# Kernel optimization log

Hardware: AMD Instinct MI355X
Metric: run time of the kernel (lower is better)

The kernel has to match this reference:

```python
import jax, jax.numpy as jnp
import numpy as np


def setup_inputs() -> dict:
    key = jax.random.key(0)
    ks = jax.random.split(key, 11)
    B, H, P, D, E = 64, 20, 448, 64, 1280
    s = 0.02
    return {
        "hidden_states": jax.random.normal(ks[0], (B, 1, E), jnp.float32),
        "past_k": jax.random.normal(ks[1], (B, H, P, D), jnp.float32),
        "past_v": jax.random.normal(ks[2], (B, H, P, D), jnp.float32),
        "past_keep_mask": jnp.zeros((1, 1, 1, P), jnp.float32),
        "Wq": jax.random.normal(ks[3], (E, E), jnp.float32) * s,
        "bq": jax.random.normal(ks[4], (E,), jnp.float32) * s,
        "Wk": jax.random.normal(ks[5], (E, E), jnp.float32) * s,
        "Wv": jax.random.normal(ks[6], (E, E), jnp.float32) * s,
        "bv": jax.random.normal(ks[7], (E,), jnp.float32) * s,
        "Wo": jax.random.normal(ks[8], (E, E), jnp.float32) * s,
        "bo": jax.random.normal(ks[9], (E,), jnp.float32) * s,
    }


def reference(hidden_states, past_k, past_v, past_keep_mask, Wq, bq, Wk, Wv, bv, Wo, bo):
    B, S, E = hidden_states.shape  # S == 1 (decode step)
    H, D = past_k.shape[1], past_k.shape[3]
    scale = jnp.asarray(D, jnp.float32) ** -0.5

    def split_heads(x):  # [B,S,E] -> [B,H,S,D]
        return x.reshape(B, S, H, D).transpose(0, 2, 1, 3)

    q = split_heads((hidden_states @ Wq.T + bq) * scale)
    new_k = split_heads(hidden_states @ Wk.T)
    new_v = split_heads(hidden_states @ Wv.T + bv)

    all_k = jnp.concatenate([past_k, new_k], axis=2)  # [B,H,P+1,D]
    all_v = jnp.concatenate([past_v, new_v], axis=2)
    mask = jnp.concatenate(
        [past_keep_mask, jnp.zeros((1, 1, 1, 1), past_keep_mask.dtype)], axis=-1
    )  # [1,1,1,P+1]

    attn = jnp.einsum("bhqd,bhkd->bhqk", q, all_k) + mask
    attn = jax.nn.softmax(attn, axis=-1)
    ctx = jnp.einsum("bhqk,bhkd->bhqd", attn, all_v)  # [B,H,S,D]
    merged = ctx.transpose(0, 2, 1, 3).reshape(B, S, E)
    out = merged @ Wo.T + bo
    return out, new_k, new_v
```

## Files before the change

### kernel.cpp

```cpp
#include <hip/hip_runtime.h>

#define EDIM 1280
#define BDIM 64
#define HDIM 20
#define PDIM 448
#define DDIM 64
#define NCOL 3840
#define NCHUNK 4
#define ECHUNK 320
#define CTILE 32

__device__ __forceinline__ float dot4(float4 a, float4 b) {
    return a.x * b.x + a.y * b.y + a.z * b.z + a.w * b.w;
}

__global__ __launch_bounds__(256) void proj_qkv(
    const float* __restrict__ h,
    const float* __restrict__ Wq, const float* __restrict__ Wk,
    const float* __restrict__ Wv,
    float* __restrict__ partial)
{
    __shared__ float Wt[CTILE * ECHUNK];

    const int wave = threadIdx.x >> 6;
    const int lane = threadIdx.x & 63;
    const int colbase = blockIdx.x * CTILE;
    const int e0 = blockIdx.y * ECHUNK;

    const float* W; int wc;
    if (colbase < EDIM)          { W = Wq; wc = colbase; }
    else if (colbase < 2 * EDIM) { W = Wk; wc = colbase - EDIM; }
    else                         { W = Wv; wc = colbase - 2 * EDIM; }

#pragma unroll
    for (int i = 0; i < 10; ++i) {
        int i4 = (i * 256 + threadIdx.x) * 4;
        int c  = i4 / ECHUNK;
        int e  = i4 - c * ECHUNK;
        *reinterpret_cast<float4*>(&Wt[i4]) =
            *reinterpret_cast<const float4*>(&W[(size_t)(wc + c) * EDIM + e0 + e]);
    }
    __syncthreads();

    float acc[8];
#pragma unroll
    for (int c = 0; c < 8; ++c) acc[c] = 0.f;

    const float4* hp = reinterpret_cast<const float4*>(h + lane * EDIM + e0);
    const int c0 = wave * 8;
#pragma unroll 4
    for (int eg = 0; eg < ECHUNK / 4; ++eg) {
        float4 hv = hp[eg];
#pragma unroll
        for (int c = 0; c < 8; ++c) {
            float4 wv = *reinterpret_cast<const float4*>(&Wt[(c0 + c) * ECHUNK + eg * 4]);
            acc[c] += dot4(hv, wv);
        }
    }
#pragma unroll
    for (int c = 0; c < 8; ++c)
        partial[((size_t)blockIdx.y * NCOL + colbase + c0 + c) * 64 + lane] = acc[c];
}

__global__ __launch_bounds__(256) void reduce_proj(
    const float* __restrict__ partial,
    const float* __restrict__ bq, const float* __restrict__ bv,
    float* __restrict__ qout, float* __restrict__ kout, float* __restrict__ vout)
{
    __shared__ float tile[256];
    const int cg0 = blockIdx.x * 4;
    const int idx = cg0 * 64 + threadIdx.x;
    float v = partial[idx] + partial[245760 + idx]
            + partial[491520 + idx] + partial[737280 + idx];
    tile[threadIdx.x] = v;
    __syncthreads();
    const int row = threadIdx.x >> 2;
    const int c   = threadIdx.x & 3;
    const int cg  = cg0 + c;
    const float v2 = tile[c * 64 + row];
    if (cg < EDIM)
        qout[row * EDIM + cg] = (v2 + bq[cg]) * 0.125f;
    else if (cg < 2 * EDIM)
        kout[row * EDIM + (cg - EDIM)] = v2;
    else
        vout[row * EDIM + (cg - 2 * EDIM)] = v2 + bv[cg - 2 * EDIM];
}

__global__ __launch_bounds__(256) void attn_decode(
    const float* __restrict__ q,
    const float* __restrict__ Kpast,
    const float* __restrict__ Vpast,
    const float* __restrict__ mask,
    const float* __restrict__ knew,
    const float* __restrict__ vnew,
    float* __restrict__ merged)
{
    __shared__ float sp[PDIM + 2];
    __shared__ float red[8];
    __shared__ float4 ctxp[4][16];

    const int bh = blockIdx.x;
    const int b  = bh / HDIM;
    const int hh = bh % HDIM;
    const int t  = threadIdx.x;
    const int w  = t >> 6;
    const int lane = t & 63;
    const int grp = t >> 4;
    const int dg  = t & 15;

    const float* qp = q + b * EDIM + hh * DDIM;
    const float* Kb = Kpast + (size_t)bh * PDIM * DDIM;
    const float* Vb = Vpast + (size_t)bh * PDIM * DDIM;
    const float* nk = knew + b * EDIM + hh * DDIM;
    const float* nv = vnew + b * EDIM + hh * DDIM;

    const float4 qv = *reinterpret_cast<const float4*>(qp + dg * 4);

    float lmax = -3.4e38f;
    for (int j0 = 0; j0 < PDIM; j0 += 64) {
        const int j = j0 + grp;
        float4 k0 = *reinterpret_cast<const float4*>(Kb + (size_t)j * DDIM + dg * 4);
        float4 k1 = *reinterpret_cast<const float4*>(Kb + (size_t)(j + 16) * DDIM + dg * 4);
        float4 k2 = *reinterpret_cast<const float4*>(Kb + (size_t)(j + 32) * DDIM + dg * 4);
        float4 k3 = *reinterpret_cast<const float4*>(Kb + (size_t)(j + 48) * DDIM + dg * 4);
        float s0 = dot4(qv, k0), s1 = dot4(qv, k1), s2 = dot4(qv, k2), s3 = dot4(qv, k3);
#pragma unroll
        for (int off = 8; off; off >>= 1) {
            s0 += __shfl_xor(s0, off, 16);
            s1 += __shfl_xor(s1, off, 16);
            s2 += __shfl_xor(s2, off, 16);
            s3 += __shfl_xor(s3, off, 16);
        }
        if (dg == 0) {
            s0 += mask[j]; s1 += mask[j + 16]; s2 += mask[j + 32]; s3 += mask[j + 48];
            sp[j] = s0; sp[j + 16] = s1; sp[j + 32] = s2; sp[j + 48] = s3;
            lmax = fmaxf(lmax, fmaxf(fmaxf(s0, s1), fmaxf(s2, s3)));
        }
    }
    if (grp == 0) {
        float4 kn = *reinterpret_cast<const float4*>(nk + dg * 4);
        float sn = dot4(qv, kn);
#pragma unroll
        for (int off = 8; off; off >>= 1) sn += __shfl_xor(sn, off, 16);
        if (dg == 0) { sp[PDIM] = sn; lmax = fmaxf(lmax, sn); }
    }
#pragma unroll
    for (int off = 32; off; off >>= 1) lmax = fmaxf(lmax, __shfl_xor(lmax, off, 64));
    if (lane == 0) red[w] = lmax;
    __syncthreads();
    const float mx = fmaxf(fmaxf(red[0], red[1]), fmaxf(red[2], red[3]));

    float lsum = 0.f;
    for (int j = t; j <= PDIM; j += 256) {
        float pj = __expf(sp[j] - mx);
        sp[j] = pj;
        lsum += pj;
    }
#pragma unroll
    for (int off = 32; off; off >>= 1) lsum += __shfl_xor(lsum, off, 64);
    if (lane == 0) red[4 + w] = lsum;
    __syncthreads();
    const float inv = 1.f / (red[4] + red[5] + red[6] + red[7]);

    const int kk = lane >> 4;
    const int dp = lane & 15;
    float4 acc = make_float4(0.f, 0.f, 0.f, 0.f);
    for (int j0 = 0; j0 < PDIM; j0 += 64) {
        const int jb = j0 + w * 16 + kk;
        float p0 = sp[jb], p1 = sp[jb + 4], p2 = sp[jb + 8], p3 = sp[jb + 12];
        float4 v0 = *reinterpret_cast<const float4*>(Vb + (size_t)jb * DDIM + dp * 4);
        float4 v1 = *reinterpret_cast<const float4*>(Vb + (size_t)(jb + 4) * DDIM + dp * 4);
        float4 v2 = *reinterpret_cast<const float4*>(Vb + (size_t)(jb + 8) * DDIM + dp * 4);
        float4 v3 = *reinterpret_cast<const float4*>(Vb + (size_t)(jb + 12) * DDIM + dp * 4);
        acc.x += p0 * v0.x + p1 * v1.x + p2 * v2.x + p3 * v3.x;
        acc.y += p0 * v0.y + p1 * v1.y + p2 * v2.y + p3 * v3.y;
        acc.z += p0 * v0.z + p1 * v1.z + p2 * v2.z + p3 * v3.z;
        acc.w += p0 * v0.w + p1 * v1.w + p2 * v2.w + p3 * v3.w;
    }
    if (w == 0 && kk == 0) {
        float pn = sp[PDIM];
        float4 vn = *reinterpret_cast<const float4*>(nv + dp * 4);
        acc.x += pn * vn.x; acc.y += pn * vn.y; acc.z += pn * vn.z; acc.w += pn * vn.w;
    }
    acc.x += __shfl_xor(acc.x, 16, 64); acc.y += __shfl_xor(acc.y, 16, 64);
    acc.z += __shfl_xor(acc.z, 16, 64); acc.w += __shfl_xor(acc.w, 16, 64);
    acc.x += __shfl_xor(acc.x, 32, 64); acc.y += __shfl_xor(acc.y, 32, 64);
    acc.z += __shfl_xor(acc.z, 32, 64); acc.w += __shfl_xor(acc.w, 32, 64);
    if (kk == 0) ctxp[w][dp] = acc;
    __syncthreads();
    if (t < 16) {
        float4 a0 = ctxp[0][t], a1 = ctxp[1][t], a2 = ctxp[2][t], a3 = ctxp[3][t];
        float4 r;
        r.x = (a0.x + a1.x + a2.x + a3.x) * inv;
        r.y = (a0.y + a1.y + a2.y + a3.y) * inv;
        r.z = (a0.z + a1.z + a2.z + a3.z) * inv;
        r.w = (a0.w + a1.w + a2.w + a3.w) * inv;
        *reinterpret_cast<float4*>(merged + b * EDIM + hh * DDIM + t * 4) = r;
    }
}

__global__ __launch_bounds__(256) void proj_out(
    const float* __restrict__ x,
    const float* __restrict__ Wo,
    float* __restrict__ partial)
{
    __shared__ float Wt[CTILE * ECHUNK];

    const int wave = threadIdx.x >> 6;
    const int lane = threadIdx.x & 63;
    const int colbase = blockIdx.x * CTILE;
    const int e0 = blockIdx.y * ECHUNK;

#pragma unroll
    for (int i = 0; i < 10; ++i) {
        int i4 = (i * 256 + threadIdx.x) * 4;
        int c  = i4 / ECHUNK;
        int e  = i4 - c * ECHUNK;
        *reinterpret_cast<float4*>(&Wt[i4]) =
            *reinterpret_cast<const float4*>(&Wo[(size_t)(colbase + c) * EDIM + e0 + e]);
    }
    __syncthreads();

    float acc[8];
#pragma unroll
    for (int c = 0; c < 8; ++c) acc[c] = 0.f;

    const float4* xp = reinterpret_cast<const float4*>(x + lane * EDIM + e0);
    const int c0 = wave * 8;
#pragma unroll 4
    for (int eg = 0; eg < ECHUNK / 4; ++eg) {
        float4 hv = xp[eg];
#pragma unroll
        for (int c = 0; c < 8; ++c) {
            float4 wv = *reinterpret_cast<const float4*>(&Wt[(c0 + c) * ECHUNK + eg * 4]);
            acc[c] += dot4(hv, wv);
        }
    }
#pragma unroll
    for (int c = 0; c < 8; ++c)
        partial[((size_t)blockIdx.y * EDIM + colbase + c0 + c) * 64 + lane] = acc[c];
}

__global__ __launch_bounds__(256) void reduce_out(
    const float* __restrict__ partial, const float* __restrict__ bo,
    float* __restrict__ out)
{
    __shared__ float tile[256];
    const int cg0 = blockIdx.x * 4;
    const int idx = cg0 * 64 + threadIdx.x;
    float v = partial[idx] + partial[81920 + idx]
            + partial[163840 + idx] + partial[245760 + idx];
    tile[threadIdx.x] = v;
    __syncthreads();
    const int row = threadIdx.x >> 2;
    const int c   = threadIdx.x & 3;
    const int cg  = cg0 + c;
    out[row * EDIM + cg] = tile[c * 64 + row] + bo[cg];
}

extern "C" void kernel_launch(void* const* d_in, const int* in_sizes, int n_in,
                              void* d_out, int out_size, void* d_ws, size_t ws_size,
                              hipStream_t stream)
{
    const float* h    = (const float*)d_in[0];
    const float* pk   = (const float*)d_in[1];
    const float* pv   = (const float*)d_in[2];
    const float* mask = (const float*)d_in[3];
    const float* Wq   = (const float*)d_in[4];
    const float* bq   = (const float*)d_in[5];
    const float* Wk   = (const float*)d_in[6];
    const float* Wv   = (const float*)d_in[7];
    const float* bv   = (const float*)d_in[8];
    const float* Wo   = (const float*)d_in[9];
    const float* bo   = (const float*)d_in[10];

    float* out  = (float*)d_out;
    float* kout = (float*)d_out + 81920;
    float* vout = (float*)d_out + 163840;

    float* ws    = (float*)d_ws;
    float* partP = ws;
    float* qbuf  = ws + 983040;
    float* mrg   = ws + 983040 + 81920;
    float* partO = ws + 983040 + 163840;

    proj_qkv<<<dim3(NCOL / CTILE, NCHUNK), 256, 0, stream>>>(h, Wq, Wk, Wv, partP);
    reduce_proj<<<dim3(NCOL / 4), 256, 0, stream>>>(partP, bq, bv, qbuf, kout, vout);
    attn_decode<<<dim3(BDIM * HDIM), 256, 0, stream>>>(qbuf, pk, pv, mask, kout, vout, mrg);
    proj_out<<<dim3(EDIM / CTILE, NCHUNK), 256, 0, stream>>>(mrg, Wo, partO);
    reduce_out<<<dim3(EDIM / 4), 256, 0, stream>>>(partO, bo, out);
}
```

Measured before the change: 97.30 us.

## Split decode attention into KV chunks with separate softmax combine kernel

Attention over the 448-entry past is split into 7 chunks of 64 keys, one block per (chunk, batch-head). Each block loads its K and V rows up front, computes a local max, exp-sum and unnormalized context, and writes them to workspace. A new combine kernel merges the chunk partials with the new-token score using log-sum-exp rescaling. This exposes seven times more blocks and more loads in flight to hide HBM latency, at the cost of an extra launch and a small partial-buffer round trip. The partial buffers reuse the projection workspace region.

```diff
diff --git a/kernel.cpp b/kernel.cpp
--- a/kernel.cpp
+++ b/kernel.cpp
@@ -9,6 +9,7 @@
 #define NCHUNK 4
 #define ECHUNK 320
 #define CTILE 32
+#define KCHUNKS 7
 
 __device__ __forceinline__ float dot4(float4 a, float4 b) {
     return a.x * b.x + a.y * b.y + a.z * b.z + a.w * b.w;
@@ -86,20 +87,20 @@
         vout[row * EDIM + (cg - 2 * EDIM)] = v2 + bv[cg - 2 * EDIM];
 }
 
-__global__ __launch_bounds__(256) void attn_decode(
+__global__ __launch_bounds__(256) void attn_part(
     const float* __restrict__ q,
     const float* __restrict__ Kpast,
     const float* __restrict__ Vpast,
     const float* __restrict__ mask,
-    const float* __restrict__ knew,
-    const float* __restrict__ vnew,
-    float* __restrict__ merged)
-{
-    __shared__ float sp[PDIM + 2];
-    __shared__ float red[8];
+    float* __restrict__ ctxbuf,
+    float* __restrict__ msbuf)
+{
+    __shared__ float redm[4];
+    __shared__ float reds[4];
     __shared__ float4 ctxp[4][16];
 
-    const int bh = blockIdx.x;
+    const int chunk = blockIdx.x;
+    const int bh    = blockIdx.y;
     const int b  = bh / HDIM;
     const int hh = bh % HDIM;
     const int t  = threadIdx.x;
@@ -108,95 +109,111 @@
     const int grp = t >> 4;
     const int dg  = t & 15;
 
-    const float* qp = q + b * EDIM + hh * DDIM;
-    const float* Kb = Kpast + (size_t)bh * PDIM * DDIM;
-    const float* Vb = Vpast + (size_t)bh * PDIM * DDIM;
-    const float* nk = knew + b * EDIM + hh * DDIM;
-    const float* nv = vnew + b * EDIM + hh * DDIM;
-
-    const float4 qv = *reinterpret_cast<const float4*>(qp + dg * 4);
-
-    float lmax = -3.4e38f;
-    for (int j0 = 0; j0 < PDIM; j0 += 64) {
-        const int j = j0 + grp;
-        float4 k0 = *reinterpret_cast<const float4*>(Kb + (size_t)j * DDIM + dg * 4);
-        float4 k1 = *reinterpret_cast<const float4*>(Kb + (size_t)(j + 16) * DDIM + dg * 4);
-        float4 k2 = *reinterpret_cast<const float4*>(Kb + (size_t)(j + 32) * DDIM + dg * 4);
-        float4 k3 = *reinterpret_cast<const float4*>(Kb + (size_t)(j + 48) * DDIM + dg * 4);
-        float s0 = dot4(qv, k0), s1 = dot4(qv, k1), s2 = dot4(qv, k2), s3 = dot4(qv, k3);
-#pragma unroll
-        for (int off = 8; off; off >>= 1) {
-            s0 += __shfl_xor(s0, off, 16);
-            s1 += __shfl_xor(s1, off, 16);
-            s2 += __shfl_xor(s2, off, 16);
-            s3 += __shfl_xor(s3, off, 16);
-        }
-        if (dg == 0) {
-            s0 += mask[j]; s1 += mask[j + 16]; s2 += mask[j + 32]; s3 += mask[j + 48];
-            sp[j] = s0; sp[j + 16] = s1; sp[j + 32] = s2; sp[j + 48] = s3;
-            lmax = fmaxf(lmax, fmaxf(fmaxf(s0, s1), fmaxf(s2, s3)));
-        }
-    }
-    if (grp == 0) {
-        float4 kn = *reinterpret_cast<const float4*>(nk + dg * 4);
-        float sn = dot4(qv, kn);
-#pragma unroll
-        for (int off = 8; off; off >>= 1) sn += __shfl_xor(sn, off, 16);
-        if (dg == 0) { sp[PDIM] = sn; lmax = fmaxf(lmax, sn); }
-    }
-#pragma unroll
-    for (int off = 32; off; off >>= 1) lmax = fmaxf(lmax, __shfl_xor(lmax, off, 64));
-    if (lane == 0) red[w] = lmax;
-    __syncthreads();
-    const float mx = fmaxf(fmaxf(red[0], red[1]), fmaxf(red[2], red[3]));
-
-    float lsum = 0.f;
-    for (int j = t; j <= PDIM; j += 256) {
-        float pj = __expf(sp[j] - mx);
-        sp[j] = pj;
-        lsum += pj;
-    }
-#pragma unroll
-    for (int off = 32; off; off >>= 1) lsum += __shfl_xor(lsum, off, 64);
-    if (lane == 0) red[4 + w] = lsum;
-    __syncthreads();
-    const float inv = 1.f / (red[4] + red[5] + red[6] + red[7]);
-
-    const int kk = lane >> 4;
-    const int dp = lane & 15;
-    float4 acc = make_float4(0.f, 0.f, 0.f, 0.f);
-    for (int j0 = 0; j0 < PDIM; j0 += 64) {
-        const int jb = j0 + w * 16 + kk;
-        float p0 = sp[jb], p1 = sp[jb + 4], p2 = sp[jb + 8], p3 = sp[jb + 12];
-        float4 v0 = *reinterpret_cast<const float4*>(Vb + (size_t)jb * DDIM + dp * 4);
-        float4 v1 = *reinterpret_cast<const float4*>(Vb + (size_t)(jb + 4) * DDIM + dp * 4);
-        float4 v2 = *reinterpret_cast<const float4*>(Vb + (size_t)(jb + 8) * DDIM + dp * 4);
-        float4 v3 = *reinterpret_cast<const float4*>(Vb + (size_t)(jb + 12) * DDIM + dp * 4);
-        acc.x += p0 * v0.x + p1 * v1.x + p2 * v2.x + p3 * v3.x;
-        acc.y += p0 * v0.y + p1 * v1.y + p2 * v2.y + p3 * v3.y;
-        acc.z += p0 * v0.z + p1 * v1.z + p2 * v2.z + p3 * v3.z;
-        acc.w += p0 * v0.w + p1 * v1.w + p2 * v2.w + p3 * v3.w;
-    }
-    if (w == 0 && kk == 0) {
-        float pn = sp[PDIM];
-        float4 vn = *reinterpret_cast<const float4*>(nv + dp * 4);
-        acc.x += pn * vn.x; acc.y += pn * vn.y; acc.z += pn * vn.z; acc.w += pn * vn.w;
-    }
+    const int j0 = chunk * 64 + grp;
+    const size_t rowbase = ((size_t)bh * PDIM + j0) * DDIM + dg * 4;
+    const float* Kr = Kpast + rowbase;
+    const float* Vr = Vpast + rowbase;
+
+    float4 k0 = *reinterpret_cast<const float4*>(Kr);
+    float4 k1 = *reinterpret_cast<const float4*>(Kr + 16 * DDIM);
+    float4 k2 = *reinterpret_cast<const float4*>(Kr + 32 * DDIM);
+    float4 k3 = *reinterpret_cast<const float4*>(Kr + 48 * DDIM);
+    float4 v0 = *reinterpret_cast<const float4*>(Vr);
+    float4 v1 = *reinterpret_cast<const float4*>(Vr + 16 * DDIM);
+    float4 v2 = *reinterpret_cast<const float4*>(Vr + 32 * DDIM);
+    float4 v3 = *reinterpret_cast<const float4*>(Vr + 48 * DDIM);
+    const float4 qv = *reinterpret_cast<const float4*>(q + b * EDIM + hh * DDIM + dg * 4);
+
+    float s0 = dot4(qv, k0), s1 = dot4(qv, k1), s2 = dot4(qv, k2), s3 = dot4(qv, k3);
+#pragma unroll
+    for (int off = 8; off; off >>= 1) {
+        s0 += __shfl_xor(s0, off, 16);
+        s1 += __shfl_xor(s1, off, 16);
+        s2 += __shfl_xor(s2, off, 16);
+        s3 += __shfl_xor(s3, off, 16);
+    }
+    s0 += mask[j0]; s1 += mask[j0 + 16]; s2 += mask[j0 + 32]; s3 += mask[j0 + 48];
+
+    float m4 = fmaxf(fmaxf(s0, s1), fmaxf(s2, s3));
+    m4 = fmaxf(m4, __shfl_xor(m4, 16, 64));
+    m4 = fmaxf(m4, __shfl_xor(m4, 32, 64));
+    if (lane == 0) redm[w] = m4;
+    __syncthreads();
+    const float mx = fmaxf(fmaxf(redm[0], redm[1]), fmaxf(redm[2], redm[3]));
+
+    float p0 = __expf(s0 - mx), p1 = __expf(s1 - mx);
+    float p2 = __expf(s2 - mx), p3 = __expf(s3 - mx);
+    float ls = p0 + p1 + p2 + p3;
+    ls += __shfl_xor(ls, 16, 64);
+    ls += __shfl_xor(ls, 32, 64);
+
+    float4 acc;
+    acc.x = p0 * v0.x + p1 * v1.x + p2 * v2.x + p3 * v3.x;
+    acc.y = p0 * v0.y + p1 * v1.y + p2 * v2.y + p3 * v3.y;
+    acc.z = p0 * v0.z + p1 * v1.z + p2 * v2.z + p3 * v3.z;
+    acc.w = p0 * v0.w + p1 * v1.w + p2 * v2.w + p3 * v3.w;
     acc.x += __shfl_xor(acc.x, 16, 64); acc.y += __shfl_xor(acc.y, 16, 64);
     acc.z += __shfl_xor(acc.z, 16, 64); acc.w += __shfl_xor(acc.w, 16, 64);
     acc.x += __shfl_xor(acc.x, 32, 64); acc.y += __shfl_xor(acc.y, 32, 64);
     acc.z += __shfl_xor(acc.z, 32, 64); acc.w += __shfl_xor(acc.w, 32, 64);
-    if (kk == 0) ctxp[w][dp] = acc;
-    __syncthreads();
+
+    if (lane == 0) reds[w] = ls;
+    if (lane < 16) ctxp[w][lane] = acc;
+    __syncthreads();
+
     if (t < 16) {
         float4 a0 = ctxp[0][t], a1 = ctxp[1][t], a2 = ctxp[2][t], a3 = ctxp[3][t];
         float4 r;
-        r.x = (a0.x + a1.x + a2.x + a3.x) * inv;
-        r.y = (a0.y + a1.y + a2.y + a3.y) * inv;
-        r.z = (a0.z + a1.z + a2.z + a3.z) * inv;
-        r.w = (a0.w + a1.w + a2.w + a3.w) * inv;
-        *reinterpret_cast<float4*>(merged + b * EDIM + hh * DDIM + t * 4) = r;
-    }
+        r.x = a0.x + a1.x + a2.x + a3.x;
+        r.y = a0.y + a1.y + a2.y + a3.y;
+        r.z = a0.z + a1.z + a2.z + a3.z;
+        r.w = a0.w + a1.w + a2.w + a3.w;
+        *reinterpret_cast<float4*>(ctxbuf + ((size_t)bh * KCHUNKS + chunk) * 64 + t * 4) = r;
+    }
+    if (t == 0) {
+        msbuf[((size_t)bh * KCHUNKS + chunk) * 2 + 0] = mx;
+        msbuf[((size_t)bh * KCHUNKS + chunk) * 2 + 1] = reds[0] + reds[1] + reds[2] + reds[3];
+    }
+}
+
+__global__ __launch_bounds__(256) void attn_combine(
+    const float* __restrict__ q,
+    const float* __restrict__ knew,
+    const float* __restrict__ vnew,
+    const float* __restrict__ ctxbuf,
+    const float* __restrict__ msbuf,
+    float* __restrict__ merged)
+{
+    const int unit = blockIdx.x * 4 + (threadIdx.x >> 6);
+    const int lane = threadIdx.x & 63;
+    const int b  = unit / HDIM;
+    const int hh = unit % HDIM;
+
+    float mc[KCHUNKS], sc[KCHUNKS];
+    float M = -3.4e38f;
+#pragma unroll
+    for (int c = 0; c < KCHUNKS; ++c) {
+        mc[c] = msbuf[((size_t)unit * KCHUNKS + c) * 2 + 0];
+        sc[c] = msbuf[((size_t)unit * KCHUNKS + c) * 2 + 1];
+        M = fmaxf(M, mc[c]);
+    }
+
+    const int base = b * EDIM + hh * DDIM + lane;
+    float sn = q[base] * knew[base];
+#pragma unroll
+    for (int off = 32; off; off >>= 1) sn += __shfl_xor(sn, off, 64);
+
+    const float M2 = fmaxf(M, sn);
+    const float pn = __expf(sn - M2);
+    float S   = pn;
+    float ctx = pn * vnew[base];
+#pragma unroll
+    for (int c = 0; c < KCHUNKS; ++c) {
+        float e = __expf(mc[c] - M2);
+        S   += sc[c] * e;
+        ctx += e * ctxbuf[((size_t)unit * KCHUNKS + c) * 64 + lane];
+    }
+    merged[base] = ctx / S;
 }
 
 __global__ __launch_bounds__(256) void proj_out(
@@ -280,13 +297,16 @@
 
     float* ws    = (float*)d_ws;
     float* partP = ws;
+    float* ctxb  = ws;
+    float* msb   = ws + 573440;
     float* qbuf  = ws + 983040;
     float* mrg   = ws + 983040 + 81920;
     float* partO = ws + 983040 + 163840;
 
     proj_qkv<<<dim3(NCOL / CTILE, NCHUNK), 256, 0, stream>>>(h, Wq, Wk, Wv, partP);
     reduce_proj<<<dim3(NCOL / 4), 256, 0, stream>>>(partP, bq, bv, qbuf, kout, vout);
-    attn_decode<<<dim3(BDIM * HDIM), 256, 0, stream>>>(qbuf, pk, pv, mask, kout, vout, mrg);
+    attn_part<<<dim3(KCHUNKS, BDIM * HDIM), 256, 0, stream>>>(qbuf, pk, pv, mask, ctxb, msb);
+    attn_combine<<<dim3(BDIM * HDIM / 4), 256, 0, stream>>>(qbuf, kout, vout, ctxb, msb, mrg);
     proj_out<<<dim3(EDIM / CTILE, NCHUNK), 256, 0, stream>>>(mrg, Wo, partO);
     reduce_out<<<dim3(EDIM / 4), 256, 0, stream>>>(partO, bo, out);
 }
```

Result: slower. 100.7 us (+3.5%).

## Fuse attention into single-pass online softmax with async K prefetch to LDS

Applied to the files above, without the earlier changes.

Rewrites the decode attention kernel as one pass using an online softmax, so K and V are consumed in the same loop instead of in separate score and context passes. K tiles are double-buffered into shared memory with global_load_lds DMA, while V is loaded directly from global memory in the same iteration. The new token's contribution and the merge of per-wave running max and sum are folded in at the end. The aim is to overlap the K and V streams and cut synchronisation phases, at the cost of 34KB of LDS per block, hand-placed waitcnt and barrier ordering, and more exp work per element.

```diff
diff --git a/kernel.cpp b/kernel.cpp
--- a/kernel.cpp
+++ b/kernel.cpp
@@ -9,9 +9,26 @@
 #define NCHUNK 4
 #define ECHUNK 320
 #define CTILE 32
+#define NTILE 7
 
 __device__ __forceinline__ float dot4(float4 a, float4 b) {
     return a.x * b.x + a.y * b.y + a.z * b.z + a.w * b.w;
+}
+
+__device__ __forceinline__ void dma16(const float* g, float* l) {
+    __builtin_amdgcn_global_load_lds(
+        (const __attribute__((address_space(1))) void*)(g),
+        (__attribute__((address_space(3))) void*)(l),
+        16, 0, 0);
+}
+
+__device__ __forceinline__ void dma_tile(const float* tbase, float* lbase,
+                                         int w, int lane) {
+#pragma unroll
+    for (int r = 0; r < 4; ++r) {
+        dma16(tbase + (size_t)(r * 256 + w * 64 + lane) * 4,
+              lbase + (r * 256 + w * 64) * 4);
+    }
 }
 
 __global__ __launch_bounds__(256) void proj_qkv(
@@ -86,7 +103,7 @@
         vout[row * EDIM + (cg - 2 * EDIM)] = v2 + bv[cg - 2 * EDIM];
 }
 
-__global__ __launch_bounds__(256) void attn_decode(
+__global__ __launch_bounds__(256, 4) void attn_fused(
     const float* __restrict__ q,
     const float* __restrict__ Kpast,
     const float* __restrict__ Vpast,
@@ -95,9 +112,10 @@
     const float* __restrict__ vnew,
     float* __restrict__ merged)
 {
-    __shared__ float sp[PDIM + 2];
-    __shared__ float red[8];
-    __shared__ float4 ctxp[4][16];
+    __shared__ __align__(16) float kbuf[2][64 * 64];
+    __shared__ __align__(16) float smask[PDIM];
+    __shared__ float4 ctxw[4][16];
+    __shared__ float mw[4], sw[4];
 
     const int bh = blockIdx.x;
     const int b  = bh / HDIM;
@@ -108,22 +126,46 @@
     const int grp = t >> 4;
     const int dg  = t & 15;
 
-    const float* qp = q + b * EDIM + hh * DDIM;
     const float* Kb = Kpast + (size_t)bh * PDIM * DDIM;
     const float* Vb = Vpast + (size_t)bh * PDIM * DDIM;
-    const float* nk = knew + b * EDIM + hh * DDIM;
-    const float* nv = vnew + b * EDIM + hh * DDIM;
-
-    const float4 qv = *reinterpret_cast<const float4*>(qp + dg * 4);
-
-    float lmax = -3.4e38f;
-    for (int j0 = 0; j0 < PDIM; j0 += 64) {
-        const int j = j0 + grp;
-        float4 k0 = *reinterpret_cast<const float4*>(Kb + (size_t)j * DDIM + dg * 4);
-        float4 k1 = *reinterpret_cast<const float4*>(Kb + (size_t)(j + 16) * DDIM + dg * 4);
-        float4 k2 = *reinterpret_cast<const float4*>(Kb + (size_t)(j + 32) * DDIM + dg * 4);
-        float4 k3 = *reinterpret_cast<const float4*>(Kb + (size_t)(j + 48) * DDIM + dg * 4);
-        float s0 = dot4(qv, k0), s1 = dot4(qv, k1), s2 = dot4(qv, k2), s3 = dot4(qv, k3);
+    const int qbase = b * EDIM + hh * DDIM;
+
+    if (t < 224) {
+        float2 mv = *reinterpret_cast<const float2*>(mask + t * 2);
+        *reinterpret_cast<float2*>(&smask[t * 2]) = mv;
+    }
+    const float4 qv = *reinterpret_cast<const float4*>(q + qbase + dg * 4);
+
+    dma_tile(Kb, kbuf[0], w, lane);
+    dma_tile(Kb + 4096, kbuf[1], w, lane);
+
+    float4 acc = make_float4(0.f, 0.f, 0.f, 0.f);
+    float Sp = 0.f;
+    float M  = -3.4e38f;
+
+#pragma unroll
+    for (int c = 0; c < NTILE; ++c) {
+        if (c < NTILE - 1) {
+            asm volatile("s_waitcnt vmcnt(4) lgkmcnt(0)" ::: "memory");
+        } else {
+            asm volatile("s_waitcnt vmcnt(0) lgkmcnt(0)" ::: "memory");
+        }
+        __builtin_amdgcn_s_barrier();
+        __builtin_amdgcn_sched_barrier(0);
+
+        const float* Vt = Vb + (size_t)(c * 64 + grp) * DDIM + dg * 4;
+        float4 v0 = *reinterpret_cast<const float4*>(Vt);
+        float4 v1 = *reinterpret_cast<const float4*>(Vt + 16 * DDIM);
+        float4 v2 = *reinterpret_cast<const float4*>(Vt + 32 * DDIM);
+        float4 v3 = *reinterpret_cast<const float4*>(Vt + 48 * DDIM);
+
+        const float* kb = kbuf[c & 1];
+        float4 k0 = *reinterpret_cast<const float4*>(kb + grp * DDIM + dg * 4);
+        float4 k1 = *reinterpret_cast<const float4*>(kb + (grp + 16) * DDIM + dg * 4);
+        float4 k2 = *reinterpret_cast<const float4*>(kb + (grp + 32) * DDIM + dg * 4);
+        float4 k3 = *reinterpret_cast<const float4*>(kb + (grp + 48) * DDIM + dg * 4);
+        float s0 = dot4(qv, k0), s1 = dot4(qv, k1);
+        float s2 = dot4(qv, k2), s3 = dot4(qv, k3);
 #pragma unroll
         for (int off = 8; off; off >>= 1) {
             s0 += __shfl_xor(s0, off, 16);
@@ -131,71 +173,63 @@
             s2 += __shfl_xor(s2, off, 16);
             s3 += __shfl_xor(s3, off, 16);
         }
-        if (dg == 0) {
-            s0 += mask[j]; s1 += mask[j + 16]; s2 += mask[j + 32]; s3 += mask[j + 48];
-            sp[j] = s0; sp[j + 16] = s1; sp[j + 32] = s2; sp[j + 48] = s3;
-            lmax = fmaxf(lmax, fmaxf(fmaxf(s0, s1), fmaxf(s2, s3)));
-        }
-    }
-    if (grp == 0) {
-        float4 kn = *reinterpret_cast<const float4*>(nk + dg * 4);
-        float sn = dot4(qv, kn);
-#pragma unroll
-        for (int off = 8; off; off >>= 1) sn += __shfl_xor(sn, off, 16);
-        if (dg == 0) { sp[PDIM] = sn; lmax = fmaxf(lmax, sn); }
-    }
-#pragma unroll
-    for (int off = 32; off; off >>= 1) lmax = fmaxf(lmax, __shfl_xor(lmax, off, 64));
-    if (lane == 0) red[w] = lmax;
-    __syncthreads();
-    const float mx = fmaxf(fmaxf(red[0], red[1]), fmaxf(red[2], red[3]));
-
-    float lsum = 0.f;
-    for (int j = t; j <= PDIM; j += 256) {
-        float pj = __expf(sp[j] - mx);
-        sp[j] = pj;
-        lsum += pj;
-    }
-#pragma unroll
-    for (int off = 32; off; off >>= 1) lsum += __shfl_xor(lsum, off, 64);
-    if (lane == 0) red[4 + w] = lsum;
-    __syncthreads();
-    const float inv = 1.f / (red[4] + red[5] + red[6] + red[7]);
-
-    const int kk = lane >> 4;
-    const int dp = lane & 15;
-    float4 acc = make_float4(0.f, 0.f, 0.f, 0.f);
-    for (int j0 = 0; j0 < PDIM; j0 += 64) {
-        const int jb = j0 + w * 16 + kk;
-        float p0 = sp[jb], p1 = sp[jb + 4], p2 = sp[jb + 8], p3 = sp[jb + 12];
-        float4 v0 = *reinterpret_cast<const float4*>(Vb + (size_t)jb * DDIM + dp * 4);
-        float4 v1 = *reinterpret_cast<const float4*>(Vb + (size_t)(jb + 4) * DDIM + dp * 4);
-        float4 v2 = *reinterpret_cast<const float4*>(Vb + (size_t)(jb + 8) * DDIM + dp * 4);
-        float4 v3 = *reinterpret_cast<const float4*>(Vb + (size_t)(jb + 12) * DDIM + dp * 4);
-        acc.x += p0 * v0.x + p1 * v1.x + p2 * v2.x + p3 * v3.x;
-        acc.y += p0 * v0.y + p1 * v1.y + p2 * v2.y + p3 * v3.y;
-        acc.z += p0 * v0.z + p1 * v1.z + p2 * v2.z + p3 * v3.z;
-        acc.w += p0 * v0.w + p1 * v1.w + p2 * v2.w + p3 * v3.w;
-    }
-    if (w == 0 && kk == 0) {
-        float pn = sp[PDIM];
-        float4 vn = *reinterpret_cast<const float4*>(nv + dp * 4);
-        acc.x += pn * vn.x; acc.y += pn * vn.y; acc.z += pn * vn.z; acc.w += pn * vn.w;
-    }
+        s0 += smask[c * 64 + grp];
+        s1 += smask[c * 64 + grp + 16];
+        s2 += smask[c * 64 + grp + 32];
+        s3 += smask[c * 64 + grp + 48];
+
+        float m4 = fmaxf(fmaxf(s0, s1), fmaxf(s2, s3));
+        m4 = fmaxf(m4, __shfl_xor(m4, 16, 64));
+        m4 = fmaxf(m4, __shfl_xor(m4, 32, 64));
+        const float newM = fmaxf(M, m4);
+        const float sc = __expf(M - newM);
+        M = newM;
+
+        const float p0 = __expf(s0 - M), p1 = __expf(s1 - M);
+        const float p2 = __expf(s2 - M), p3 = __expf(s3 - M);
+        Sp = Sp * sc + (p0 + p1 + p2 + p3);
+        acc.x = acc.x * sc + p0 * v0.x + p1 * v1.x + p2 * v2.x + p3 * v3.x;
+        acc.y = acc.y * sc + p0 * v0.y + p1 * v1.y + p2 * v2.y + p3 * v3.y;
+        acc.z = acc.z * sc + p0 * v0.z + p1 * v1.z + p2 * v2.z + p3 * v3.z;
+        acc.w = acc.w * sc + p0 * v0.w + p1 * v1.w + p2 * v2.w + p3 * v3.w;
+
+        asm volatile("s_waitcnt lgkmcnt(0)" ::: "memory");
+        __builtin_amdgcn_s_barrier();
+        __builtin_amdgcn_sched_barrier(0);
+        if (c + 2 < NTILE)
+            dma_tile(Kb + (size_t)(c + 2) * 4096, kbuf[c & 1], w, lane);
+    }
+
     acc.x += __shfl_xor(acc.x, 16, 64); acc.y += __shfl_xor(acc.y, 16, 64);
     acc.z += __shfl_xor(acc.z, 16, 64); acc.w += __shfl_xor(acc.w, 16, 64);
     acc.x += __shfl_xor(acc.x, 32, 64); acc.y += __shfl_xor(acc.y, 32, 64);
     acc.z += __shfl_xor(acc.z, 32, 64); acc.w += __shfl_xor(acc.w, 32, 64);
-    if (kk == 0) ctxp[w][dp] = acc;
-    __syncthreads();
+    Sp += __shfl_xor(Sp, 16, 64);
+    Sp += __shfl_xor(Sp, 32, 64);
+    if (lane < 16) ctxw[w][lane] = acc;
+    if (lane == 0) { mw[w] = M; sw[w] = Sp; }
+    __syncthreads();
+
     if (t < 16) {
-        float4 a0 = ctxp[0][t], a1 = ctxp[1][t], a2 = ctxp[2][t], a3 = ctxp[3][t];
+        float4 knv = *reinterpret_cast<const float4*>(knew + qbase + t * 4);
+        float4 vnv = *reinterpret_cast<const float4*>(vnew + qbase + t * 4);
+        float4 qv2 = *reinterpret_cast<const float4*>(q + qbase + t * 4);
+        float sn = dot4(qv2, knv);
+#pragma unroll
+        for (int off = 8; off; off >>= 1) sn += __shfl_xor(sn, off, 16);
+
+        const float Mf = fmaxf(fmaxf(fmaxf(mw[0], mw[1]), fmaxf(mw[2], mw[3])), sn);
+        const float e0 = __expf(mw[0] - Mf), e1 = __expf(mw[1] - Mf);
+        const float e2 = __expf(mw[2] - Mf), e3 = __expf(mw[3] - Mf);
+        const float en = __expf(sn - Mf);
+        const float S = sw[0] * e0 + sw[1] * e1 + sw[2] * e2 + sw[3] * e3 + en;
+        const float4 c0 = ctxw[0][t], c1 = ctxw[1][t], c2 = ctxw[2][t], c3 = ctxw[3][t];
         float4 r;
-        r.x = (a0.x + a1.x + a2.x + a3.x) * inv;
-        r.y = (a0.y + a1.y + a2.y + a3.y) * inv;
-        r.z = (a0.z + a1.z + a2.z + a3.z) * inv;
-        r.w = (a0.w + a1.w + a2.w + a3.w) * inv;
-        *reinterpret_cast<float4*>(merged + b * EDIM + hh * DDIM + t * 4) = r;
+        r.x = (c0.x * e0 + c1.x * e1 + c2.x * e2 + c3.x * e3 + en * vnv.x) / S;
+        r.y = (c0.y * e0 + c1.y * e1 + c2.y * e2 + c3.y * e3 + en * vnv.y) / S;
+        r.z = (c0.z * e0 + c1.z * e1 + c2.z * e2 + c3.z * e3 + en * vnv.z) / S;
+        r.w = (c0.w * e0 + c1.w * e1 + c2.w * e2 + c3.w * e3 + en * vnv.w) / S;
+        *reinterpret_cast<float4*>(merged + qbase + t * 4) = r;
     }
 }
 
@@ -286,7 +320,7 @@
 
     proj_qkv<<<dim3(NCOL / CTILE, NCHUNK), 256, 0, stream>>>(h, Wq, Wk, Wv, partP);
     reduce_proj<<<dim3(NCOL / 4), 256, 0, stream>>>(partP, bq, bv, qbuf, kout, vout);
-    attn_decode<<<dim3(BDIM * HDIM), 256, 0, stream>>>(qbuf, pk, pv, mask, kout, vout, mrg);
+    attn_fused<<<dim3(BDIM * HDIM), 256, 0, stream>>>(qbuf, pk, pv, mask, kout, vout, mrg);
     proj_out<<<dim3(EDIM / CTILE, NCHUNK), 256, 0, stream>>>(mrg, Wo, partO);
     reduce_out<<<dim3(EDIM / 4), 256, 0, stream>>>(partO, bo, out);
 }
```

Measured after the change: 130.2 us. 1.34x slower.
